# Kernel optimization log

Measured on AMD Instinct MI355X. Metric: run time of the kernel, lower is better.

Reference implementation:

```python
import jax, jax.numpy as jnp
import numpy as np

DIM = 512
HIDDEN = 2048
D_M = 256
R = 64
GEN_HIDDEN = D_M * 2  # hidden_mul=2
ALPHA_MEM = 1.0


def setup_inputs() -> dict:
    key = jax.random.key(0)
    ks = jax.random.split(key, 12)
    B, T = 2, 512
    inp = {
        'x': jax.random.normal(ks[0], (B, T, DIM), jnp.float32),
        'm_tok': jax.random.normal(ks[1], (B, T, D_M), jnp.float32),
        # base SwiGLU params
        'W1': jax.random.normal(ks[2], (HIDDEN, DIM), jnp.float32) * (1.0 / np.sqrt(DIM)),
        'W2': jax.random.normal(ks[3], (HIDDEN, DIM), jnp.float32) * (1.0 / np.sqrt(DIM)),
        'W3': jax.random.normal(ks[4], (DIM, HIDDEN), jnp.float32) * (1.0 / np.sqrt(HIDDEN)),
        'b1': jnp.zeros((HIDDEN,), jnp.float32),
        'b2': jnp.zeros((HIDDEN,), jnp.float32),
        'b3': jnp.zeros((DIM,), jnp.float32),
        # hypernetwork (FFNMemGenerator): d_m -> gen_hidden -> 3*r*dim
        'gen_w1': jax.random.normal(ks[5], (GEN_HIDDEN, D_M), jnp.float32) * (1.0 / np.sqrt(D_M)),
        'gen_b1': jnp.zeros((GEN_HIDDEN,), jnp.float32),
        'gen_w2': jax.random.normal(ks[6], (3 * R * DIM, GEN_HIDDEN), jnp.float32) * (0.02 / np.sqrt(GEN_HIDDEN)),
        'gen_b2': jnp.zeros((3 * R * DIM,), jnp.float32),
        'mem_gate': jnp.zeros((), jnp.float32),
    }
    return inp


def reference(x, m_tok, W1, W2, W3, b1, b2, b3, gen_w1, gen_b1, gen_w2, gen_b2, mem_gate):
    B, T, _ = x.shape
    # base SwiGLU FFN
    x1 = jnp.einsum('od,btd->bto', W1, x) + b1  # [B,T,hidden]
    x2 = jnp.einsum('od,btd->bto', W2, x) + b2
    h_base = jax.nn.silu(x1) * x2
    y_base = jnp.einsum('do,bto->btd', W3, h_base) + b3  # [B,T,dim]

    # hypernetwork-generated per-token low-rank weights
    hg = jax.nn.silu(jnp.einsum('hd,btd->bth', gen_w1, m_tok) + gen_b1)
    w = jnp.einsum('oh,bth->bto', gen_w2, hg) + gen_b2  # [B,T,3*r*dim]
    W1_m = w[..., : R * DIM].reshape(B, T, R, DIM)
    W2_m = w[..., R * DIM : 2 * R * DIM].reshape(B, T, R, DIM)
    W3_m = w[..., 2 * R * DIM :].reshape(B, T, DIM, R)

    # per-token batched matvecs (memory path)
    u1 = jnp.einsum('btrd,btd->btr', W1_m, x)
    u2 = jnp.einsum('btrd,btd->btr', W2_m, x)
    h_mem = jax.nn.silu(u1) * u2
    y_mem = jnp.einsum('btdr,btr->btd', W3_m, h_mem)

    g = jax.nn.sigmoid(mem_gate)
    return y_base + g * ALPHA_MEM * y_mem
```

## Files before the change

kernel.cpp:

```cpp
#include <hip/hip_runtime.h>
#include <cstdint>
#include <cstddef>

#define TOK   1024
#define DIMX  512
#define HID   2048
#define DM    256
#define GENH  512
#define RR    64
#define O3BASE 65536

typedef __bf16 bf16x8 __attribute__((ext_vector_type(8)));
typedef float  f32x4  __attribute__((ext_vector_type(4)));

__device__ __forceinline__ unsigned short f2bf(float f) {
  union { float f; uint32_t u; } v; v.f = f;
  return (unsigned short)((v.u + 0x7fffu + ((v.u >> 16) & 1u)) >> 16);
}
__device__ __forceinline__ float bf2f(unsigned short h) {
  union { uint32_t u; float f; } v; v.u = (uint32_t)h << 16;
  return v.f;
}
__device__ __forceinline__ float silu_f(float x) { return x / (1.f + __expf(-x)); }

__device__ __forceinline__ void async_copy16(const void* g, void* l) {
  __builtin_amdgcn_global_load_lds(
      (const __attribute__((address_space(1))) void*)g,
      (__attribute__((address_space(3))) void*)l, 16, 0, 0);
}

__global__ __launch_bounds__(256) void cast_bf16_kernel(
    const float* __restrict__ src, unsigned short* __restrict__ dst) {
  size_t i = ((size_t)blockIdx.x * 256 + threadIdx.x) * 8;
  float4 v0 = *(const float4*)(src + i);
  float4 v1 = *(const float4*)(src + i + 4);
  ushort4 h0, h1;
  h0.x = f2bf(v0.x); h0.y = f2bf(v0.y); h0.z = f2bf(v0.z); h0.w = f2bf(v0.w);
  h1.x = f2bf(v1.x); h1.y = f2bf(v1.y); h1.z = f2bf(v1.z); h1.w = f2bf(v1.w);
  *(ushort4*)(dst + i)     = h0;
  *(ushort4*)(dst + i + 4) = h1;
}

__device__ __forceinline__ void stage_tile(
    const unsigned short* __restrict__ base, size_t row0, int stride, int kofs,
    unsigned short* Ls, int wave, int lane) {
#pragma unroll
  for (int j = 0; j < 4; ++j) {
    int s   = wave * 256 + j * 64 + lane;
    int row = s >> 3;
    int kc  = (s & 7) ^ (row & 7);
    const unsigned short* g = base + (row0 + (size_t)row) * (size_t)stride + kofs + kc * 8;
    async_copy16(g, (char*)Ls + wave * 4096 + j * 1024);
  }
}

template<int KLEN>
__device__ __forceinline__ void mfma_tile_nt(
    const unsigned short* __restrict__ Abf, size_t a_row0, int astride,
    const unsigned short* __restrict__ Bbf, size_t b_row0, int bstride, int k0,
    unsigned short* As, unsigned short* Bs, f32x4 (&acc)[4][4]) {
  const int tid  = threadIdx.x;
  const int lane = tid & 63;
  const int wave = tid >> 6;
  const int m0 = (wave >> 1) * 64, n0 = (wave & 1) * 64;

  for (int kk = 0; kk < KLEN; kk += 64) {
    stage_tile(Abf, a_row0, astride, k0 + kk, As, wave, lane);
    stage_tile(Bbf, b_row0, bstride, k0 + kk, Bs, wave, lane);
    __syncthreads();
#pragma unroll
    for (int ks = 0; ks < 2; ++ks) {
      int cbase = ks * 4 + (lane >> 4);
      int koff  = (cbase ^ (lane & 7)) * 8;
      bf16x8 a[4], b[4];
#pragma unroll
      for (int mf = 0; mf < 4; ++mf)
        a[mf] = *(const bf16x8*)(As + (m0 + mf * 16 + (lane & 15)) * 64 + koff);
#pragma unroll
      for (int nf = 0; nf < 4; ++nf)
        b[nf] = *(const bf16x8*)(Bs + (n0 + nf * 16 + (lane & 15)) * 64 + koff);
#pragma unroll
      for (int mf = 0; mf < 4; ++mf)
#pragma unroll
        for (int nf = 0; nf < 4; ++nf)
          acc[mf][nf] = __builtin_amdgcn_mfma_f32_16x16x32_bf16(
              a[mf], b[nf], acc[mf][nf], 0, 0, 0);
    }
    __syncthreads();
  }
}

__device__ __forceinline__ void zero_acc(f32x4 (&acc)[4][4]) {
#pragma unroll
  for (int i = 0; i < 4; ++i)
#pragma unroll
    for (int j = 0; j < 4; ++j) {
      f32x4 z = {0.f, 0.f, 0.f, 0.f};
      acc[i][j] = z;
    }
}

__global__ __launch_bounds__(256) void prep_kernel(
    const float* __restrict__ x, const float* __restrict__ m_tok,
    const float* __restrict__ gen_w1, const float* __restrict__ gen_b1,
    unsigned short* __restrict__ xb, unsigned short* __restrict__ hgb) {
  __shared__ float mt[4 * DM];
  const int tid = threadIdx.x;
  const size_t t0 = (size_t)blockIdx.x * 4;
#pragma unroll
  for (int k = 0; k < 4; ++k) mt[k * 256 + tid] = m_tok[t0 * DM + k * 256 + tid];
#pragma unroll
  for (int k = 0; k < 8; ++k) {
    size_t idx = t0 * DIMX + k * 256 + tid;
    xb[idx] = f2bf(x[idx]);
  }
  __syncthreads();
#pragma unroll
  for (int hh = 0; hh < 2; ++hh) {
    int h = hh * 256 + tid;
    float a0, a1, a2, a3;
    a0 = a1 = a2 = a3 = gen_b1[h];
    const float* wr = gen_w1 + (size_t)h * DM;
    for (int d = 0; d < DM; d += 4) {
      float4 w = *(const float4*)(wr + d);
      a0 += w.x * mt[d]       + w.y * mt[d + 1]       + w.z * mt[d + 2]       + w.w * mt[d + 3];
      a1 += w.x * mt[256 + d] + w.y * mt[256 + d + 1] + w.z * mt[256 + d + 2] + w.w * mt[256 + d + 3];
      a2 += w.x * mt[512 + d] + w.y * mt[512 + d + 1] + w.z * mt[512 + d + 2] + w.w * mt[512 + d + 3];
      a3 += w.x * mt[768 + d] + w.y * mt[768 + d + 1] + w.z * mt[768 + d + 2] + w.w * mt[768 + d + 3];
    }
    hgb[(t0 + 0) * GENH + h] = f2bf(silu_f(a0));
    hgb[(t0 + 1) * GENH + h] = f2bf(silu_f(a1));
    hgb[(t0 + 2) * GENH + h] = f2bf(silu_f(a2));
    hgb[(t0 + 3) * GENH + h] = f2bf(silu_f(a3));
  }
}

template<int N, int KFULL, int KTILE, bool SPLIT>
__global__ __launch_bounds__(256) void gemm_nt_kernel(
    const unsigned short* __restrict__ A, const unsigned short* __restrict__ B,
    const float* __restrict__ bias, float* __restrict__ C) {
  __shared__ unsigned short As[8192];
  __shared__ unsigned short Bs[8192];
  constexpr int NB = N / 128;
  const int ob = blockIdx.x % NB, tb = blockIdx.x / NB;
  const size_t o0 = (size_t)ob * 128, t0 = (size_t)tb * 128;
  const int k0 = SPLIT ? blockIdx.y * KTILE : 0;
  f32x4 acc[4][4];
  zero_acc(acc);
  mfma_tile_nt<KTILE>(A, t0, KFULL, B, o0, KFULL, k0, As, Bs, acc);

  const int tid = threadIdx.x, lane = tid & 63, wave = tid >> 6;
  const int m0 = (wave >> 1) * 64, n0 = (wave & 1) * 64;
#pragma unroll
  for (int nf = 0; nf < 4; ++nf) {
    int n = n0 + nf * 16 + (lane & 15);
    float bv = (!SPLIT || k0 == 0) ? bias[o0 + n] : 0.f;
#pragma unroll
    for (int mf = 0; mf < 4; ++mf) {
      int mb = m0 + mf * 16 + ((lane >> 4) << 2);
#pragma unroll
      for (int rg = 0; rg < 4; ++rg) {
        size_t idx = (t0 + mb + rg) * (size_t)N + o0 + n;
        float v = acc[mf][nf][rg] + bv;
        if (SPLIT) atomicAdd(&C[idx], v);
        else C[idx] = v;
      }
    }
  }
}

__global__ void silu_mul_kernel(const float* __restrict__ a,
                                const float* __restrict__ b,
                                unsigned short* __restrict__ o) {
  size_t i = (size_t)blockIdx.x * 256 + threadIdx.x;
  o[i] = f2bf(silu_f(a[i]) * b[i]);
}

union SmemUV {
  struct { unsigned short As[8192], Bs[8192]; } ab;
  struct { unsigned short Xs[128 * 132]; float upart[128]; } ep;
};

__global__ __launch_bounds__(256) void memuv_kernel(
    const unsigned short* __restrict__ hgb, const unsigned short* __restrict__ w2b,
    const float* __restrict__ gen_b2, const unsigned short* __restrict__ xb,
    float* __restrict__ u) {
  __shared__ SmemUV sm;
  const int bx = blockIdx.x;
  const int tb = bx & 7, ob = bx >> 3;
  const size_t o0 = (size_t)ob * 128, t0 = (size_t)tb * 128;
  const int j  = ob >> 2;
  const int d0 = (ob & 3) * 128;

  f32x4 acc[4][4];
  zero_acc(acc);
  mfma_tile_nt<GENH>(hgb, t0, GENH, w2b, o0, GENH, 0, sm.ab.As, sm.ab.Bs, acc);

  const int tid = threadIdx.x, lane = tid & 63, wave = tid >> 6;
#pragma unroll
  for (int i = 0; i < 8; ++i) {
    int q = i * 256 + tid;
    int row = q >> 4, c = q & 15;
    const unsigned short* src = xb + (t0 + (size_t)row) * DIMX + d0 + c * 8;
    ushort4 v0 = *(const ushort4*)src;
    ushort4 v1 = *(const ushort4*)(src + 4);
    unsigned short* dst = sm.ep.Xs + row * 132 + c * 8;
    *(ushort4*)dst = v0;
    *(ushort4*)(dst + 4) = v1;
  }
  if (tid < 128) sm.ep.upart[tid] = 0.f;
  __syncthreads();

  const int m0 = (wave >> 1) * 64, n0 = (wave & 1) * 64;
  float gb[4];
#pragma unroll
  for (int nf = 0; nf < 4; ++nf)
    gb[nf] = gen_b2[o0 + n0 + nf * 16 + (lane & 15)];
#pragma unroll
  for (int mf = 0; mf < 4; ++mf) {
    int rb = m0 + mf * 16 + ((lane >> 4) << 2);
#pragma unroll
    for (int rg = 0; rg < 4; ++rg) {
      int trow = rb + rg;
      float val = 0.f;
#pragma unroll
      for (int nf = 0; nf < 4; ++nf) {
        int col = n0 + nf * 16 + (lane & 15);
        val += (acc[mf][nf][rg] + gb[nf]) * bf2f(sm.ep.Xs[trow * 132 + col]);
      }
      val += __shfl_xor(val, 1);
      val += __shfl_xor(val, 2);
      val += __shfl_xor(val, 4);
      val += __shfl_xor(val, 8);
      if ((lane & 15) == 0) atomicAdd(&sm.ep.upart[trow], val);
    }
  }
  __syncthreads();
  if (tid < 128) atomicAdd(&u[(t0 + tid) * 128 + j], sm.ep.upart[tid]);
}

__global__ void hmem_kernel(const float* __restrict__ u, float* __restrict__ hm) {
  int i = blockIdx.x * 256 + threadIdx.x;
  int t = i >> 6, r = i & 63;
  float u1 = u[t * 128 + r], u2 = u[t * 128 + 64 + r];
  hm[i] = silu_f(u1) * u2;
}

union SmemY {
  struct { unsigned short As[8192], Bs[8192]; } ab;
  struct { float Hs[128 * 66]; float ypart[256]; } ep;
};

__global__ __launch_bounds__(256) void memy_kernel(
    const unsigned short* __restrict__ hgb, const unsigned short* __restrict__ w2b,
    const float* __restrict__ gen_b2, const float* __restrict__ hmem,
    const float* __restrict__ mem_gate, float* __restrict__ y) {
  __shared__ SmemY sm;
  const int bx = blockIdx.x;
  const int tb = bx & 7, ob = bx >> 3;
  const size_t brow0 = (size_t)O3BASE + (size_t)ob * 128;
  const size_t t0 = (size_t)tb * 128;

  f32x4 acc[4][4];
  zero_acc(acc);
  mfma_tile_nt<GENH>(hgb, t0, GENH, w2b, brow0, GENH, 0, sm.ab.As, sm.ab.Bs, acc);

  const int tid = threadIdx.x, lane = tid & 63, wave = tid >> 6;
#pragma unroll
  for (int i = 0; i < 8; ++i) {
    int q = i * 256 + tid;
    int row = q >> 4, c = q & 15;
    float4 v = *(const float4*)(hmem + (t0 + (size_t)row) * RR + c * 4);
    float* dst = sm.ep.Hs + row * 66 + c * 4;
    *(float2*)dst = make_float2(v.x, v.y);
    *(float2*)(dst + 2) = make_float2(v.z, v.w);
  }
  sm.ep.ypart[tid] = 0.f;
  __syncthreads();

  const int m0 = (wave >> 1) * 64, n0 = (wave & 1) * 64;
  const int dsel = n0 >> 6;
  float gb[4];
#pragma unroll
  for (int nf = 0; nf < 4; ++nf)
    gb[nf] = gen_b2[brow0 + n0 + nf * 16 + (lane & 15)];
#pragma unroll
  for (int mf = 0; mf < 4; ++mf) {
    int rb = m0 + mf * 16 + ((lane >> 4) << 2);
#pragma unroll
    for (int rg = 0; rg < 4; ++rg) {
      int trow = rb + rg;
      float val = 0.f;
#pragma unroll
      for (int nf = 0; nf < 4; ++nf) {
        int r = nf * 16 + (lane & 15);
        val += (acc[mf][nf][rg] + gb[nf]) * sm.ep.Hs[trow * 66 + r];
      }
      val += __shfl_xor(val, 1);
      val += __shfl_xor(val, 2);
      val += __shfl_xor(val, 4);
      val += __shfl_xor(val, 8);
      if ((lane & 15) == 0) atomicAdd(&sm.ep.ypart[trow * 2 + dsel], val);
    }
  }
  __syncthreads();
  {
    float g = 1.f / (1.f + __expf(-mem_gate[0]));
    int t = tid >> 1, di = tid & 1;
    size_t gi = (t0 + (size_t)t) * DIMX + (size_t)ob * 2 + di;
    y[gi] += g * sm.ep.ypart[t * 2 + di];
  }
}

extern "C" void kernel_launch(void* const* d_in, const int* in_sizes, int n_in,
                              void* d_out, int out_size, void* d_ws, size_t ws_size,
                              hipStream_t stream) {
  const float* x        = (const float*)d_in[0];
  const float* m_tok    = (const float*)d_in[1];
  const float* W1       = (const float*)d_in[2];
  const float* W2       = (const float*)d_in[3];
  const float* W3       = (const float*)d_in[4];
  const float* b1       = (const float*)d_in[5];
  const float* b2       = (const float*)d_in[6];
  const float* b3       = (const float*)d_in[7];
  const float* gen_w1   = (const float*)d_in[8];
  const float* gen_b1   = (const float*)d_in[9];
  const float* gen_w2   = (const float*)d_in[10];
  const float* gen_b2   = (const float*)d_in[11];
  const float* mem_gate = (const float*)d_in[12];
  float* y = (float*)d_out;

  char* ws = (char*)d_ws;
#define MB(v) ((size_t)(v) << 20)
  unsigned short* xb  = (unsigned short*)(ws);
  unsigned short* hgb = (unsigned short*)(ws + MB(1));
  float* x1 = (float*)(ws + MB(2));
  float* x2 = (float*)(ws + MB(10));
  unsigned short* hb  = (unsigned short*)(ws + MB(18));
  float* u  = (float*)(ws + MB(22));
  float* hm = (float*)(ws + MB(22) + (512u << 10));
  unsigned short* W1b = (unsigned short*)(ws + MB(23));
  unsigned short* W2b = (unsigned short*)(ws + MB(25));
  unsigned short* W3b = (unsigned short*)(ws + MB(27));
  unsigned short* w2b = (unsigned short*)(ws + MB(29));
#undef MB

  prep_kernel<<<256, 256, 0, stream>>>(x, m_tok, gen_w1, gen_b1, xb, hgb);
  cast_bf16_kernel<<<24576, 256, 0, stream>>>(gen_w2, w2b);
  cast_bf16_kernel<<<512, 256, 0, stream>>>(W1, W1b);
  cast_bf16_kernel<<<512, 256, 0, stream>>>(W2, W2b);
  cast_bf16_kernel<<<512, 256, 0, stream>>>(W3, W3b);
  hipMemsetAsync(u, 0, TOK * 128 * sizeof(float), stream);
  hipMemsetAsync(y, 0, (size_t)out_size * sizeof(float), stream);

  gemm_nt_kernel<HID, DIMX, DIMX, false><<<dim3(16 * 8), 256, 0, stream>>>(xb, W1b, b1, x1);
  gemm_nt_kernel<HID, DIMX, DIMX, false><<<dim3(16 * 8), 256, 0, stream>>>(xb, W2b, b2, x2);
  silu_mul_kernel<<<(TOK * HID) / 256, 256, 0, stream>>>(x1, x2, hb);
  gemm_nt_kernel<DIMX, HID, DIMX, true><<<dim3(4 * 8, 4), 256, 0, stream>>>(hb, W3b, b3, y);

  memuv_kernel<<<512 * 8, 256, 0, stream>>>(hgb, w2b, gen_b2, xb, u);
  hmem_kernel<<<(TOK * RR) / 256, 256, 0, stream>>>(u, hm);
  memy_kernel<<<256 * 8, 256, 0, stream>>>(hgb, w2b, gen_b2, hm, mem_gate, y);
}
```

Baseline: 581.7 us.

## Fuse SwiGLU GEMMs, drop atomics and memsets, fold weight casts into prep

Merges the W1 and W2 GEMMs and the silu-mul into one kernel that writes bf16 h directly, removing the two fp32 intermediate buffers. The split-K W3 GEMM and the memory-path reductions now write partial sums to separate buffers instead of using atomics. memy_kernel adds those partials, b3 and the gated memory term into y in one store, so both memsets go away. The three base weight casts are folded into prep_kernel to cut launches. This costs extra partial-sum traffic and a heavier memy epilogue, and the dominant gen_w2 cast and hypernetwork GEMMs are left unchanged.

After: 1.064 ms. +82.9%, slower.

```diff
diff --git a/kernel.cpp b/kernel.cpp
--- a/kernel.cpp
+++ b/kernel.cpp
@@ -29,9 +29,8 @@
       (__attribute__((address_space(3))) void*)l, 16, 0, 0);
 }
 
-__global__ __launch_bounds__(256) void cast_bf16_kernel(
-    const float* __restrict__ src, unsigned short* __restrict__ dst) {
-  size_t i = ((size_t)blockIdx.x * 256 + threadIdx.x) * 8;
+__device__ __forceinline__ void cast8(const float* __restrict__ src,
+                                      unsigned short* __restrict__ dst, size_t i) {
   float4 v0 = *(const float4*)(src + i);
   float4 v1 = *(const float4*)(src + i + 4);
   ushort4 h0, h1;
@@ -41,16 +40,24 @@
   *(ushort4*)(dst + i + 4) = h1;
 }
 
+__global__ __launch_bounds__(256) void cast_bf16_kernel(
+    const float* __restrict__ src, unsigned short* __restrict__ dst) {
+  cast8(src, dst, ((size_t)blockIdx.x * 256 + threadIdx.x) * 8);
+}
+
+template<int ROWS>
 __device__ __forceinline__ void stage_tile(
     const unsigned short* __restrict__ base, size_t row0, int stride, int kofs,
-    unsigned short* Ls, int wave, int lane) {
-#pragma unroll
-  for (int j = 0; j < 4; ++j) {
-    int s   = wave * 256 + j * 64 + lane;
+    unsigned short* Ls, int tid) {
+  constexpr int IT = ROWS / 32;
+  const int wave = tid >> 6, lane = tid & 63;
+#pragma unroll
+  for (int j = 0; j < IT; ++j) {
+    int s   = wave * (IT * 64) + j * 64 + lane;
     int row = s >> 3;
     int kc  = (s & 7) ^ (row & 7);
     const unsigned short* g = base + (row0 + (size_t)row) * (size_t)stride + kofs + kc * 8;
-    async_copy16(g, (char*)Ls + wave * 4096 + j * 1024);
+    async_copy16(g, (char*)Ls + wave * (IT * 1024) + j * 1024);
   }
 }
 
@@ -65,8 +72,8 @@
   const int m0 = (wave >> 1) * 64, n0 = (wave & 1) * 64;
 
   for (int kk = 0; kk < KLEN; kk += 64) {
-    stage_tile(Abf, a_row0, astride, k0 + kk, As, wave, lane);
-    stage_tile(Bbf, b_row0, bstride, k0 + kk, Bs, wave, lane);
+    stage_tile<128>(Abf, a_row0, astride, k0 + kk, As, tid);
+    stage_tile<128>(Bbf, b_row0, bstride, k0 + kk, Bs, tid);
     __syncthreads();
 #pragma unroll
     for (int ks = 0; ks < 2; ++ks) {
@@ -90,7 +97,7 @@
   }
 }
 
-__device__ __forceinline__ void zero_acc(f32x4 (&acc)[4][4]) {
+__device__ __forceinline__ void zero_acc4(f32x4 (&acc)[4][4]) {
 #pragma unroll
   for (int i = 0; i < 4; ++i)
 #pragma unroll
@@ -103,7 +110,11 @@
 __global__ __launch_bounds__(256) void prep_kernel(
     const float* __restrict__ x, const float* __restrict__ m_tok,
     const float* __restrict__ gen_w1, const float* __restrict__ gen_b1,
-    unsigned short* __restrict__ xb, unsigned short* __restrict__ hgb) {
+    const float* __restrict__ W1, const float* __restrict__ W2,
+    const float* __restrict__ W3,
+    unsigned short* __restrict__ xb, unsigned short* __restrict__ hgb,
+    unsigned short* __restrict__ W1b, unsigned short* __restrict__ W2b,
+    unsigned short* __restrict__ W3b) {
   __shared__ float mt[4 * DM];
   const int tid = threadIdx.x;
   const size_t t0 = (size_t)blockIdx.x * 4;
@@ -113,6 +124,16 @@
   for (int k = 0; k < 8; ++k) {
     size_t idx = t0 * DIMX + k * 256 + tid;
     xb[idx] = f2bf(x[idx]);
+  }
+  {
+    size_t base = ((size_t)blockIdx.x * 256 + tid) * 8;
+#pragma unroll
+    for (int it = 0; it < 2; ++it) {
+      size_t idx = base + (size_t)it * 524288;
+      cast8(W1, W1b, idx);
+      cast8(W2, W2b, idx);
+      cast8(W3, W3b, idx);
+    }
   }
   __syncthreads();
 #pragma unroll
@@ -135,56 +156,114 @@
   }
 }
 
-template<int N, int KFULL, int KTILE, bool SPLIT>
-__global__ __launch_bounds__(256) void gemm_nt_kernel(
-    const unsigned short* __restrict__ A, const unsigned short* __restrict__ B,
-    const float* __restrict__ bias, float* __restrict__ C) {
+__global__ __launch_bounds__(256) void ffn12_kernel(
+    const unsigned short* __restrict__ xb, const unsigned short* __restrict__ W1b,
+    const unsigned short* __restrict__ W2b, const float* __restrict__ pb1,
+    const float* __restrict__ pb2, unsigned short* __restrict__ hb) {
+  __shared__ unsigned short As[64 * 64];
+  __shared__ unsigned short B1s[128 * 64];
+  __shared__ unsigned short B2s[128 * 64];
+  const int tid = threadIdx.x, lane = tid & 63, wave = tid >> 6;
+  const int ob = blockIdx.x & 15, tb = blockIdx.x >> 4;
+  const size_t t0 = (size_t)tb * 64, o0 = (size_t)ob * 128;
+  const int m0 = (wave >> 1) * 32, n0 = (wave & 1) * 64;
+
+  f32x4 acc1[2][4], acc2[2][4];
+#pragma unroll
+  for (int i = 0; i < 2; ++i)
+#pragma unroll
+    for (int j = 0; j < 4; ++j) {
+      f32x4 z = {0.f, 0.f, 0.f, 0.f};
+      acc1[i][j] = z; acc2[i][j] = z;
+    }
+
+  for (int kk = 0; kk < DIMX; kk += 64) {
+    stage_tile<64>(xb, t0, DIMX, kk, As, tid);
+    stage_tile<128>(W1b, o0, DIMX, kk, B1s, tid);
+    stage_tile<128>(W2b, o0, DIMX, kk, B2s, tid);
+    __syncthreads();
+#pragma unroll
+    for (int ks = 0; ks < 2; ++ks) {
+      int cbase = ks * 4 + (lane >> 4);
+      int koff  = (cbase ^ (lane & 7)) * 8;
+      bf16x8 a[2], b1[4], b2[4];
+#pragma unroll
+      for (int mf = 0; mf < 2; ++mf)
+        a[mf] = *(const bf16x8*)(As + (m0 + mf * 16 + (lane & 15)) * 64 + koff);
+#pragma unroll
+      for (int nf = 0; nf < 4; ++nf) {
+        b1[nf] = *(const bf16x8*)(B1s + (n0 + nf * 16 + (lane & 15)) * 64 + koff);
+        b2[nf] = *(const bf16x8*)(B2s + (n0 + nf * 16 + (lane & 15)) * 64 + koff);
+      }
+#pragma unroll
+      for (int mf = 0; mf < 2; ++mf)
+#pragma unroll
+        for (int nf = 0; nf < 4; ++nf) {
+          acc1[mf][nf] = __builtin_amdgcn_mfma_f32_16x16x32_bf16(a[mf], b1[nf], acc1[mf][nf], 0, 0, 0);
+          acc2[mf][nf] = __builtin_amdgcn_mfma_f32_16x16x32_bf16(a[mf], b2[nf], acc2[mf][nf], 0, 0, 0);
+        }
+    }
+    __syncthreads();
+  }
+
+  const int q = lane >> 4;
+  float b1v[4], b2v[4];
+#pragma unroll
+  for (int nf = 0; nf < 4; ++nf) {
+    b1v[nf] = pb1[o0 + n0 + nf * 16 + (lane & 15)];
+    b2v[nf] = pb2[o0 + n0 + nf * 16 + (lane & 15)];
+  }
+#pragma unroll
+  for (int mf = 0; mf < 2; ++mf)
+#pragma unroll
+    for (int nf = 0; nf < 4; ++nf)
+#pragma unroll
+      for (int rg = 0; rg < 4; ++rg) {
+        size_t trow = t0 + m0 + mf * 16 + q * 4 + rg;
+        size_t col  = o0 + n0 + nf * 16 + (lane & 15);
+        float v1 = acc1[mf][nf][rg] + b1v[nf];
+        float v2 = acc2[mf][nf][rg] + b2v[nf];
+        hb[trow * HID + col] = f2bf(silu_f(v1) * v2);
+      }
+}
+
+__global__ __launch_bounds__(256) void gemm3p_kernel(
+    const unsigned short* __restrict__ hb, const unsigned short* __restrict__ W3b,
+    float* __restrict__ yp) {
   __shared__ unsigned short As[8192];
   __shared__ unsigned short Bs[8192];
-  constexpr int NB = N / 128;
-  const int ob = blockIdx.x % NB, tb = blockIdx.x / NB;
+  const int ob = blockIdx.x & 3, tb = blockIdx.x >> 2;
   const size_t o0 = (size_t)ob * 128, t0 = (size_t)tb * 128;
-  const int k0 = SPLIT ? blockIdx.y * KTILE : 0;
+  const int k0 = blockIdx.y * 512;
   f32x4 acc[4][4];
-  zero_acc(acc);
-  mfma_tile_nt<KTILE>(A, t0, KFULL, B, o0, KFULL, k0, As, Bs, acc);
+  zero_acc4(acc);
+  mfma_tile_nt<512>(hb, t0, HID, W3b, o0, HID, k0, As, Bs, acc);
 
   const int tid = threadIdx.x, lane = tid & 63, wave = tid >> 6;
   const int m0 = (wave >> 1) * 64, n0 = (wave & 1) * 64;
+  float* out = yp + (size_t)blockIdx.y * (TOK * DIMX);
 #pragma unroll
   for (int nf = 0; nf < 4; ++nf) {
     int n = n0 + nf * 16 + (lane & 15);
-    float bv = (!SPLIT || k0 == 0) ? bias[o0 + n] : 0.f;
 #pragma unroll
     for (int mf = 0; mf < 4; ++mf) {
       int mb = m0 + mf * 16 + ((lane >> 4) << 2);
 #pragma unroll
-      for (int rg = 0; rg < 4; ++rg) {
-        size_t idx = (t0 + mb + rg) * (size_t)N + o0 + n;
-        float v = acc[mf][nf][rg] + bv;
-        if (SPLIT) atomicAdd(&C[idx], v);
-        else C[idx] = v;
-      }
-    }
-  }
-}
-
-__global__ void silu_mul_kernel(const float* __restrict__ a,
-                                const float* __restrict__ b,
-                                unsigned short* __restrict__ o) {
-  size_t i = (size_t)blockIdx.x * 256 + threadIdx.x;
-  o[i] = f2bf(silu_f(a[i]) * b[i]);
+      for (int rg = 0; rg < 4; ++rg)
+        out[(t0 + mb + rg) * DIMX + o0 + n] = acc[mf][nf][rg];
+    }
+  }
 }
 
 union SmemUV {
   struct { unsigned short As[8192], Bs[8192]; } ab;
-  struct { unsigned short Xs[128 * 132]; float upart[128]; } ep;
+  struct { unsigned short Xs[128 * 128]; } ep;
 };
 
 __global__ __launch_bounds__(256) void memuv_kernel(
     const unsigned short* __restrict__ hgb, const unsigned short* __restrict__ w2b,
     const float* __restrict__ gen_b2, const unsigned short* __restrict__ xb,
-    float* __restrict__ u) {
+    float* __restrict__ up) {
   __shared__ SmemUV sm;
   const int bx = blockIdx.x;
   const int tb = bx & 7, ob = bx >> 3;
@@ -193,7 +272,7 @@
   const int d0 = (ob & 3) * 128;
 
   f32x4 acc[4][4];
-  zero_acc(acc);
+  zero_acc4(acc);
   mfma_tile_nt<GENH>(hgb, t0, GENH, w2b, o0, GENH, 0, sm.ab.As, sm.ab.Bs, acc);
 
   const int tid = threadIdx.x, lane = tid & 63, wave = tid >> 6;
@@ -204,56 +283,60 @@
     const unsigned short* src = xb + (t0 + (size_t)row) * DIMX + d0 + c * 8;
     ushort4 v0 = *(const ushort4*)src;
     ushort4 v1 = *(const ushort4*)(src + 4);
-    unsigned short* dst = sm.ep.Xs + row * 132 + c * 8;
+    unsigned short* dst = sm.ep.Xs + row * 128 + c * 8;
     *(ushort4*)dst = v0;
     *(ushort4*)(dst + 4) = v1;
   }
-  if (tid < 128) sm.ep.upart[tid] = 0.f;
   __syncthreads();
 
   const int m0 = (wave >> 1) * 64, n0 = (wave & 1) * 64;
-  float gb[4];
-#pragma unroll
-  for (int nf = 0; nf < 4; ++nf)
-    gb[nf] = gen_b2[o0 + n0 + nf * 16 + (lane & 15)];
-#pragma unroll
-  for (int mf = 0; mf < 4; ++mf) {
-    int rb = m0 + mf * 16 + ((lane >> 4) << 2);
+  const int q = lane >> 4;
+  float gbv[4];
+#pragma unroll
+  for (int i = 0; i < 4; ++i)
+    gbv[i] = gen_b2[o0 + n0 + i * 16 + (lane & 15)];
+#pragma unroll
+  for (int mf = 0; mf < 4; ++mf)
 #pragma unroll
     for (int rg = 0; rg < 4; ++rg) {
-      int trow = rb + rg;
+      int trow = m0 + mf * 16 + q * 4 + rg;
       float val = 0.f;
 #pragma unroll
       for (int nf = 0; nf < 4; ++nf) {
-        int col = n0 + nf * 16 + (lane & 15);
-        val += (acc[mf][nf][rg] + gb[nf]) * bf2f(sm.ep.Xs[trow * 132 + col]);
+        int nfp = (nf + q) & 3;
+        int col = n0 + nfp * 16 + (lane & 15);
+        val += (acc[mf][nfp][rg] + gbv[nfp]) * bf2f(sm.ep.Xs[trow * 128 + col]);
       }
       val += __shfl_xor(val, 1);
       val += __shfl_xor(val, 2);
       val += __shfl_xor(val, 4);
       val += __shfl_xor(val, 8);
-      if ((lane & 15) == 0) atomicAdd(&sm.ep.upart[trow], val);
-    }
-  }
-  __syncthreads();
-  if (tid < 128) atomicAdd(&u[(t0 + tid) * 128 + j], sm.ep.upart[tid]);
-}
-
-__global__ void hmem_kernel(const float* __restrict__ u, float* __restrict__ hm) {
+      if ((lane & 15) == 0)
+        up[(t0 + trow) * 1024 + j * 8 + (ob & 3) * 2 + (wave & 1)] = val;
+    }
+}
+
+__global__ __launch_bounds__(256) void hmem_kernel(
+    const float* __restrict__ up, float* __restrict__ hm) {
   int i = blockIdx.x * 256 + threadIdx.x;
   int t = i >> 6, r = i & 63;
-  float u1 = u[t * 128 + r], u2 = u[t * 128 + 64 + r];
+  const float* p1 = up + (size_t)t * 1024 + r * 8;
+  const float* p2 = p1 + 512;
+  float u1 = 0.f, u2 = 0.f;
+#pragma unroll
+  for (int p = 0; p < 8; ++p) { u1 += p1[p]; u2 += p2[p]; }
   hm[i] = silu_f(u1) * u2;
 }
 
 union SmemY {
   struct { unsigned short As[8192], Bs[8192]; } ab;
-  struct { float Hs[128 * 66]; float ypart[256]; } ep;
+  struct { float Hs[128 * 64]; } ep;
 };
 
 __global__ __launch_bounds__(256) void memy_kernel(
     const unsigned short* __restrict__ hgb, const unsigned short* __restrict__ w2b,
     const float* __restrict__ gen_b2, const float* __restrict__ hmem,
+    const float* __restrict__ yp, const float* __restrict__ b3,
     const float* __restrict__ mem_gate, float* __restrict__ y) {
   __shared__ SmemY sm;
   const int bx = blockIdx.x;
@@ -262,7 +345,7 @@
   const size_t t0 = (size_t)tb * 128;
 
   f32x4 acc[4][4];
-  zero_acc(acc);
+  zero_acc4(acc);
   mfma_tile_nt<GENH>(hgb, t0, GENH, w2b, brow0, GENH, 0, sm.ab.As, sm.ab.Bs, acc);
 
   const int tid = threadIdx.x, lane = tid & 63, wave = tid >> 6;
@@ -271,45 +354,43 @@
     int q = i * 256 + tid;
     int row = q >> 4, c = q & 15;
     float4 v = *(const float4*)(hmem + (t0 + (size_t)row) * RR + c * 4);
-    float* dst = sm.ep.Hs + row * 66 + c * 4;
-    *(float2*)dst = make_float2(v.x, v.y);
-    *(float2*)(dst + 2) = make_float2(v.z, v.w);
-  }
-  sm.ep.ypart[tid] = 0.f;
+    *(float4*)(sm.ep.Hs + row * 64 + c * 4) = v;
+  }
   __syncthreads();
 
   const int m0 = (wave >> 1) * 64, n0 = (wave & 1) * 64;
-  const int dsel = n0 >> 6;
-  float gb[4];
-#pragma unroll
-  for (int nf = 0; nf < 4; ++nf)
-    gb[nf] = gen_b2[brow0 + n0 + nf * 16 + (lane & 15)];
-#pragma unroll
-  for (int mf = 0; mf < 4; ++mf) {
-    int rb = m0 + mf * 16 + ((lane >> 4) << 2);
+  const int q = lane >> 4;
+  const float g = 1.f / (1.f + __expf(-mem_gate[0]));
+  float gbv[4];
+#pragma unroll
+  for (int i = 0; i < 4; ++i)
+    gbv[i] = gen_b2[brow0 + n0 + i * 16 + (lane & 15)];
+#pragma unroll
+  for (int mf = 0; mf < 4; ++mf)
 #pragma unroll
     for (int rg = 0; rg < 4; ++rg) {
-      int trow = rb + rg;
+      int trow = m0 + mf * 16 + q * 4 + rg;
       float val = 0.f;
 #pragma unroll
       for (int nf = 0; nf < 4; ++nf) {
-        int r = nf * 16 + (lane & 15);
-        val += (acc[mf][nf][rg] + gb[nf]) * sm.ep.Hs[trow * 66 + r];
+        int nfp = (nf + q) & 3;
+        int r = nfp * 16 + (lane & 15);
+        val += (acc[mf][nfp][rg] + gbv[nfp]) * sm.ep.Hs[trow * 64 + r];
       }
       val += __shfl_xor(val, 1);
       val += __shfl_xor(val, 2);
       val += __shfl_xor(val, 4);
       val += __shfl_xor(val, 8);
-      if ((lane & 15) == 0) atomicAdd(&sm.ep.ypart[trow * 2 + dsel], val);
-    }
-  }
-  __syncthreads();
-  {
-    float g = 1.f / (1.f + __expf(-mem_gate[0]));
-    int t = tid >> 1, di = tid & 1;
-    size_t gi = (t0 + (size_t)t) * DIMX + (size_t)ob * 2 + di;
-    y[gi] += g * sm.ep.ypart[t * 2 + di];
-  }
+      if ((lane & 15) == 0) {
+        int d = ob * 2 + (wave & 1);
+        size_t t = t0 + trow;
+        float acc_y = b3[d];
+#pragma unroll
+        for (int s = 0; s < 4; ++s)
+          acc_y += yp[(size_t)s * (TOK * DIMX) + t * DIMX + d];
+        y[t * DIMX + d] = acc_y + g * val;
+      }
+    }
 }
 
 extern "C" void kernel_launch(void* const* d_in, const int* in_sizes, int n_in,
@@ -331,34 +412,27 @@
   float* y = (float*)d_out;
 
   char* ws = (char*)d_ws;
-#define MB(v) ((size_t)(v) << 20)
+#define KB(v) ((size_t)(v) << 10)
   unsigned short* xb  = (unsigned short*)(ws);
-  unsigned short* hgb = (unsigned short*)(ws + MB(1));
-  float* x1 = (float*)(ws + MB(2));
-  float* x2 = (float*)(ws + MB(10));
-  unsigned short* hb  = (unsigned short*)(ws + MB(18));
-  float* u  = (float*)(ws + MB(22));
-  float* hm = (float*)(ws + MB(22) + (512u << 10));
-  unsigned short* W1b = (unsigned short*)(ws + MB(23));
-  unsigned short* W2b = (unsigned short*)(ws + MB(25));
-  unsigned short* W3b = (unsigned short*)(ws + MB(27));
-  unsigned short* w2b = (unsigned short*)(ws + MB(29));
-#undef MB
-
-  prep_kernel<<<256, 256, 0, stream>>>(x, m_tok, gen_w1, gen_b1, xb, hgb);
+  unsigned short* hgb = (unsigned short*)(ws + KB(1024));
+  unsigned short* hb  = (unsigned short*)(ws + KB(2048));
+  float* up = (float*)(ws + KB(6144));
+  float* hm = (float*)(ws + KB(10240));
+  float* yp = (float*)(ws + KB(10752));
+  unsigned short* W1b = (unsigned short*)(ws + KB(18944));
+  unsigned short* W2b = (unsigned short*)(ws + KB(20992));
+  unsigned short* W3b = (unsigned short*)(ws + KB(23040));
+  unsigned short* w2b = (unsigned short*)(ws + KB(25088));
+#undef KB
+
+  prep_kernel<<<256, 256, 0, stream>>>(x, m_tok, gen_w1, gen_b1, W1, W2, W3,
+                                       xb, hgb, W1b, W2b, W3b);
   cast_bf16_kernel<<<24576, 256, 0, stream>>>(gen_w2, w2b);
-  cast_bf16_kernel<<<512, 256, 0, stream>>>(W1, W1b);
-  cast_bf16_kernel<<<512, 256, 0, stream>>>(W2, W2b);
-  cast_bf16_kernel<<<512, 256, 0, stream>>>(W3, W3b);
-  hipMemsetAsync(u, 0, TOK * 128 * sizeof(float), stream);
-  hipMemsetAsync(y, 0, (size_t)out_size * sizeof(float), stream);
-
-  gemm_nt_kernel<HID, DIMX, DIMX, false><<<dim3(16 * 8), 256, 0, stream>>>(xb, W1b, b1, x1);
-  gemm_nt_kernel<HID, DIMX, DIMX, false><<<dim3(16 * 8), 256, 0, stream>>>(xb, W2b, b2, x2);
-  silu_mul_kernel<<<(TOK * HID) / 256, 256, 0, stream>>>(x1, x2, hb);
-  gemm_nt_kernel<DIMX, HID, DIMX, true><<<dim3(4 * 8, 4), 256, 0, stream>>>(hb, W3b, b3, y);
-
-  memuv_kernel<<<512 * 8, 256, 0, stream>>>(hgb, w2b, gen_b2, xb, u);
-  hmem_kernel<<<(TOK * RR) / 256, 256, 0, stream>>>(u, hm);
-  memy_kernel<<<256 * 8, 256, 0, stream>>>(hgb, w2b, gen_b2, hm, mem_gate, y);
-}
+
+  ffn12_kernel<<<256, 256, 0, stream>>>(xb, W1b, W2b, b1, b2, hb);
+  gemm3p_kernel<<<dim3(32, 4), 256, 0, stream>>>(hb, W3b, yp);
+
+  memuv_kernel<<<4096, 256, 0, stream>>>(hgb, w2b, gen_b2, xb, up);
+  hmem_kernel<<<256, 256, 0, stream>>>(up, hm);
+  memy_kernel<<<2048, 256, 0, stream>>>(hgb, w2b, gen_b2, hm, yp, b3, mem_gate, y);
+}
```
